# Optimization experiments

Measured on AMD Instinct MI355X. Metric: run time of the kernel, lower is better.

The kernel has to match this reference:

```python
import jax, jax.numpy as jnp
import numpy as np


def setup_inputs() -> dict:
    key = jax.random.key(0)
    ks = jax.random.split(key, 8)
    B, C, H, W = 8, 512, 64, 64
    Cr = C // 8  # reduction=8
    s = 1.0 / np.sqrt(C)
    return {
        "x": jax.random.normal(ks[0], (B, C, H, W), jnp.float32),
        "wq": jax.random.normal(ks[1], (Cr, C), jnp.float32) * s,
        "bq": jax.random.normal(ks[2], (Cr,), jnp.float32) * 0.01,
        "wk": jax.random.normal(ks[3], (Cr, C), jnp.float32) * s,
        "bk": jax.random.normal(ks[4], (Cr,), jnp.float32) * 0.01,
        "wv": jax.random.normal(ks[5], (C, C), jnp.float32) * s,
        "bv": jax.random.normal(ks[6], (C,), jnp.float32) * 0.01,
        "gamma": jax.random.normal(ks[7], (1,), jnp.float32),
    }


def reference(x, wq, bq, wk, bk, wv, bv, gamma):
    B, C, H, W = x.shape
    N = H * W
    xf = x.reshape(B, C, N)  # 1x1 conv == channel matmul
    q = jnp.einsum('qc,bcn->bnq', wq, xf) + bq  # [B, N, Cr]
    k = jnp.einsum('qc,bcn->bqn', wk, xf) + bk[None, :, None]  # [B, Cr, N]
    v = jnp.einsum('vc,bcn->bvn', wv, xf) + bv[None, :, None]  # [B, C, N]
    energy = jnp.einsum('bnq,bqm->bnm', q, k)  # [B, N, N]
    attn = jax.nn.softmax(energy, axis=-1)
    out = jnp.einsum('bcm,bnm->bcn', v, attn)  # [B, C, N]
    out = out.reshape(B, C, H, W)
    return gamma * out + x
```

## Files before the change

kernel.cpp:

```cpp
#include <hip/hip_runtime.h>

typedef float  f32x4  __attribute__((ext_vector_type(4)));
typedef float  f32x16 __attribute__((ext_vector_type(16)));
typedef short  short8 __attribute__((ext_vector_type(8)));
typedef unsigned int uint4v __attribute__((ext_vector_type(4)));

#define LOG2E 1.4426950408889634f
#define NPIX 4096
#define CCH  512
#define DQK  64

__device__ __forceinline__ ushort f2b(float f) {
  union { float f; unsigned u; } v; v.f = f;
  unsigned r = v.u + 0x7fffu + ((v.u >> 16) & 1u);
  return (ushort)(r >> 16);
}

__device__ __forceinline__ unsigned cvt_pk_bf16(float lo, float hi) {
  unsigned r;
  asm("v_cvt_pk_bf16_f32 %0, %1, %2" : "=v"(r) : "v"(lo), "v"(hi));
  return r;
}

__device__ __forceinline__ void plane_swap(unsigned &a, unsigned &b) {
  asm volatile("v_permlane32_swap_b32 %0, %1" : "+v"(a), "+v"(b));
}

__device__ __forceinline__ void gload16(const ushort* g, ushort* l) {
  __builtin_amdgcn_global_load_lds((const __attribute__((address_space(1))) void*)g,
                                   (__attribute__((address_space(3))) void*)l, 16, 0, 0);
}

__global__ __launch_bounds__(256) void k_cast_x(const float* __restrict__ x,
                                                ushort* __restrict__ Xt) {
  __shared__ float tile[32][33];
  const int b = blockIdx.z;
  const int n0 = blockIdx.x * 32, c0 = blockIdx.y * 32;
  const int t = threadIdx.x;
  {
    int cc = t >> 3, nn = (t & 7) * 4;
    const float4 v = *(const float4*)&x[((size_t)b * CCH + c0 + cc) * NPIX + n0 + nn];
    tile[cc][nn] = v.x; tile[cc][nn + 1] = v.y; tile[cc][nn + 2] = v.z; tile[cc][nn + 3] = v.w;
  }
  __syncthreads();
  {
    int nr = t >> 3, c4 = (t & 7) * 4;
    ushort4 o;
    o.x = f2b(tile[c4 + 0][nr]); o.y = f2b(tile[c4 + 1][nr]);
    o.z = f2b(tile[c4 + 2][nr]); o.w = f2b(tile[c4 + 3][nr]);
    *(ushort4*)&Xt[((size_t)b * NPIX + n0 + nr) * CCH + c0 + c4] = o;
  }
}

__global__ __launch_bounds__(256) void k_cast_w(const float* __restrict__ wq,
                                                const float* __restrict__ wk,
                                                const float* __restrict__ wv,
                                                ushort* __restrict__ Wb) {
  int i = blockIdx.x * 256 + threadIdx.x;
  int idx = i * 4;
  int j = idx >> 9, c = idx & 511;
  const float* src = (j < 64) ? &wq[(size_t)j * 512]
                   : (j < 128) ? &wk[(size_t)(j - 64) * 512]
                               : &wv[(size_t)(j - 128) * 512];
  float4 v = *(const float4*)&src[c];
  ushort4 o; o.x = f2b(v.x); o.y = f2b(v.y); o.z = f2b(v.z); o.w = f2b(v.w);
  *(ushort4*)&Wb[idx] = o;
}

__global__ __launch_bounds__(256) void k_proj(const ushort* __restrict__ Xt,
                                              const ushort* __restrict__ Wb,
                                              const float* __restrict__ bq,
                                              const float* __restrict__ bk,
                                              const float* __restrict__ bv,
                                              ushort* __restrict__ Qf,
                                              ushort* __restrict__ Kf,
                                              ushort* __restrict__ Vf) {
  __shared__ ushort Wl[64][72];
  __shared__ ushort Xl[64][72];
  const int b = blockIdx.z;
  const int n0 = blockIdx.x * 64;
  const int j0 = blockIdx.y * 64;
  const int t = threadIdx.x;
  const int w = t >> 6, l = t & 63;
  const int lr = l & 15, lq = l >> 4;
  const int wj = (w >> 1) * 32, wn = (w & 1) * 32;

  f32x4 acc[2][2];
#pragma unroll
  for (int a = 0; a < 2; ++a)
#pragma unroll
    for (int c = 0; c < 2; ++c) acc[a][c] = f32x4{0.f, 0.f, 0.f, 0.f};

  const int srow = t >> 2, sch = t & 3;
  for (int k0 = 0; k0 < 512; k0 += 64) {
    *(uint4*)&Wl[srow][sch * 8]       = *(const uint4*)&Wb[(size_t)(j0 + srow) * 512 + k0 + sch * 8];
    *(uint4*)&Wl[srow][(sch + 4) * 8] = *(const uint4*)&Wb[(size_t)(j0 + srow) * 512 + k0 + (sch + 4) * 8];
    *(uint4*)&Xl[srow][sch * 8]       = *(const uint4*)&Xt[((size_t)b * NPIX + n0 + srow) * 512 + k0 + sch * 8];
    *(uint4*)&Xl[srow][(sch + 4) * 8] = *(const uint4*)&Xt[((size_t)b * NPIX + n0 + srow) * 512 + k0 + (sch + 4) * 8];
    __syncthreads();
#pragma unroll
    for (int kt = 0; kt < 2; ++kt) {
      short8 af[2], bf[2];
#pragma unroll
      for (int jt = 0; jt < 2; ++jt)
        af[jt] = *(const short8*)&Wl[wj + jt * 16 + lr][kt * 32 + lq * 8];
#pragma unroll
      for (int nt = 0; nt < 2; ++nt)
        bf[nt] = *(const short8*)&Xl[wn + nt * 16 + lr][kt * 32 + lq * 8];
#pragma unroll
      for (int jt = 0; jt < 2; ++jt)
#pragma unroll
        for (int nt = 0; nt < 2; ++nt)
          acc[jt][nt] = __builtin_amdgcn_mfma_f32_16x16x32_bf16(af[jt], bf[nt], acc[jt][nt], 0, 0, 0);
    }
    __syncthreads();
  }

#pragma unroll
  for (int jt = 0; jt < 2; ++jt) {
    const int jb = j0 + wj + jt * 16;
#pragma unroll
    for (int nt = 0; nt < 2; ++nt) {
      const int n = n0 + wn + nt * 16 + lr;
      const int n32 = (n0 + wn) >> 5;
      if (jb < 64) {
        const int kd0 = jb + lq * 4;
        const int ks = jb >> 4;
        const int hl = lq >> 1;
        const int e0 = (lq * 4) & 7;
        const int lp = (nt * 16 + lr) + 32 * hl;
        ushort4 o;
        o.x = f2b(LOG2E * (acc[jt][nt][0] + bq[kd0 + 0]));
        o.y = f2b(LOG2E * (acc[jt][nt][1] + bq[kd0 + 1]));
        o.z = f2b(LOG2E * (acc[jt][nt][2] + bq[kd0 + 2]));
        o.w = f2b(LOG2E * (acc[jt][nt][3] + bq[kd0 + 3]));
        *(ushort4*)&Qf[((size_t)(b * 128 + n32) * 4 + ks) * 512 + lp * 8 + e0] = o;
      } else if (jb < 128) {
        const int kd0 = jb - 64 + lq * 4;
        const int ks = (jb - 64) >> 4;
        const int hl = lq >> 1;
        const int e0 = (lq * 4) & 7;
        const int lp = (nt * 16 + lr) + 32 * hl;
        ushort4 o;
        o.x = f2b(acc[jt][nt][0] + bk[kd0 + 0]);
        o.y = f2b(acc[jt][nt][1] + bk[kd0 + 1]);
        o.z = f2b(acc[jt][nt][2] + bk[kd0 + 2]);
        o.w = f2b(acc[jt][nt][3] + bk[kd0 + 3]);
        *(ushort4*)&Kf[((size_t)(b * 128 + n32) * 4 + ks) * 512 + lp * 8 + e0] = o;
      } else {
        const int kt = nt;
        const int hlv = (lr >> 3) & 1;
        const int e = lr & 7;
#pragma unroll
        for (int r = 0; r < 4; ++r) {
          const int c = jb - 128 + lq * 4 + r;
          Vf[(((size_t)(b * 128 + n32) * 16 + (c >> 5)) * 2 + kt) * 512 +
             (c & 31) * 8 + 256 * hlv + e] = f2b(acc[jt][nt][r] + bv[c]);
        }
      }
    }
  }
}

__global__ __launch_bounds__(512, 4) void k_attn(const ushort* __restrict__ Qf,
                                                 const ushort* __restrict__ Kf,
                                                 const ushort* __restrict__ Vf,
                                                 const float* __restrict__ x,
                                                 const float* __restrict__ gamma,
                                                 float* __restrict__ out) {
  __shared__ unsigned Plds[2][8][2][2][64][2];
  __shared__ ushort Klds[2][8192];
  __shared__ ushort Qlds[4096];
  __shared__ float Lred[2][4][32];
  const int id = blockIdx.x;
  const int b  = id & 7;
  const int qb = id >> 3;
  const int t = threadIdx.x;
  const int w = t >> 6, l = t & 63;
  const int lq = l & 31, h = l >> 5;
  const int kg = w >> 1;
  const int q32p = w & 1;
  const int qw = qb * 64;

  union PB { uint4v u; short8 s8; };

  const ushort* kslice = Kf + (size_t)(b * 128) * 2048;
  const ushort* vbase  = Vf + (size_t)b * 128 * 16384 + (size_t)(2 * w) * 1024 + (size_t)l * 8;

  f32x16 acc[2][2] = {};
  float Lp = 0.f;

  auto stageK = [&](int buf, int tile) {
    const ushort* src = kslice + (size_t)tile * 8192;
#pragma unroll
    for (int i = 0; i < 2; ++i) {
      const int cb_ = i * 512 + w * 64;
      gload16(src + (size_t)(cb_ + l) * 8, &Klds[buf][cb_ * 8]);
    }
  };

  gload16(Qf + (size_t)(b * 128 + qb * 2) * 2048 + (size_t)(w * 64 + l) * 8, &Qlds[w * 512]);
  stageK(0, 0);
  __syncthreads();

  for (int tile = 0; tile < 32; ++tile) {
    const int buf = tile & 1;
    if (tile + 1 < 32) stageK(buf ^ 1, tile + 1);

    {
      const ushort* kb = &Klds[buf][(kg * 4) * 512 + l * 8];
      short8 kf0 = *(const short8*)(kb);
      short8 kf1 = *(const short8*)(kb + 512);
      short8 kf2 = *(const short8*)(kb + 1024);
      short8 kf3 = *(const short8*)(kb + 1536);
      const ushort* qp = &Qlds[q32p * 2048 + l * 8];
      short8 q0 = *(const short8*)(qp);
      short8 q1 = *(const short8*)(qp + 512);
      short8 q2 = *(const short8*)(qp + 1024);
      short8 q3 = *(const short8*)(qp + 1536);
      f32x16 s = {};
      __builtin_amdgcn_s_setprio(1);
      s = __builtin_amdgcn_mfma_f32_32x32x16_bf16(kf0, q0, s, 0, 0, 0);
      s = __builtin_amdgcn_mfma_f32_32x32x16_bf16(kf1, q1, s, 0, 0, 0);
      s = __builtin_amdgcn_mfma_f32_32x32x16_bf16(kf2, q2, s, 0, 0, 0);
      s = __builtin_amdgcn_mfma_f32_32x32x16_bf16(kf3, q3, s, 0, 0, 0);
      __builtin_amdgcn_s_setprio(0);

      float sum = 0.f;
#pragma unroll
      for (int r = 0; r < 16; ++r) { s[r] = __builtin_amdgcn_exp2f(s[r]); sum += s[r]; }
      Lp += sum;
      unsigned pk0 = cvt_pk_bf16(s[0],  s[1]),  pk1 = cvt_pk_bf16(s[2],  s[3]);
      unsigned pk2 = cvt_pk_bf16(s[4],  s[5]),  pk3 = cvt_pk_bf16(s[6],  s[7]);
      unsigned pk4 = cvt_pk_bf16(s[8],  s[9]),  pk5 = cvt_pk_bf16(s[10], s[11]);
      unsigned pk6 = cvt_pk_bf16(s[12], s[13]), pk7 = cvt_pk_bf16(s[14], s[15]);
      plane_swap(pk0, pk2); plane_swap(pk1, pk3);
      plane_swap(pk4, pk6); plane_swap(pk5, pk7);
      *(uint2*)&Plds[buf][kg * 2 + 0][q32p][0][l][0] = uint2{pk0, pk1};
      *(uint2*)&Plds[buf][kg * 2 + 0][q32p][1][l][0] = uint2{pk2, pk3};
      *(uint2*)&Plds[buf][kg * 2 + 1][q32p][0][l][0] = uint2{pk4, pk5};
      *(uint2*)&Plds[buf][kg * 2 + 1][q32p][1][l][0] = uint2{pk6, pk7};
    }
    __syncthreads();

#pragma unroll
    for (int k8 = 0; k8 < 8; ++k8) {
      const ushort* pv = vbase + (size_t)(tile * 4 + (k8 >> 1)) * 16384 + (size_t)(k8 & 1) * 512;
      short8 v0 = *(const short8*)(pv);
      short8 v1 = *(const short8*)(pv + 1024);
      uint2 a0 = *(const uint2*)&Plds[buf][k8][0][0][l][0];
      uint2 a1 = *(const uint2*)&Plds[buf][k8][0][1][l][0];
      uint2 b0 = *(const uint2*)&Plds[buf][k8][1][0][l][0];
      uint2 b1 = *(const uint2*)&Plds[buf][k8][1][1][l][0];
      PB B0, B1;
      B0.u[0] = a0.x; B0.u[1] = a0.y; B0.u[2] = a1.x; B0.u[3] = a1.y;
      B1.u[0] = b0.x; B1.u[1] = b0.y; B1.u[2] = b1.x; B1.u[3] = b1.y;
      __builtin_amdgcn_s_setprio(1);
      acc[0][0] = __builtin_amdgcn_mfma_f32_32x32x16_bf16(v0, B0.s8, acc[0][0], 0, 0, 0);
      acc[0][1] = __builtin_amdgcn_mfma_f32_32x32x16_bf16(v1, B0.s8, acc[0][1], 0, 0, 0);
      acc[1][0] = __builtin_amdgcn_mfma_f32_32x32x16_bf16(v0, B1.s8, acc[1][0], 0, 0, 0);
      acc[1][1] = __builtin_amdgcn_mfma_f32_32x32x16_bf16(v1, B1.s8, acc[1][1], 0, 0, 0);
      __builtin_amdgcn_s_setprio(0);
    }
  }

  Lp += __shfl_xor(Lp, 32);
  Lred[q32p][kg][lq] = Lp;
  __syncthreads();
  float Lt0 = (Lred[0][0][lq] + Lred[0][1][lq]) + (Lred[0][2][lq] + Lred[0][3][lq]);
  float Lt1 = (Lred[1][0][lq] + Lred[1][1][lq]) + (Lred[1][2][lq] + Lred[1][3][lq]);
  const float g = gamma[0];
  const float gi0 = g / Lt0, gi1 = g / Lt1;
#pragma unroll
  for (int ct = 0; ct < 2; ++ct)
#pragma unroll
    for (int r = 0; r < 16; ++r) {
      const int c = w * 64 + ct * 32 + (r & 3) + 8 * (r >> 2) + 4 * h;
      const size_t base = ((size_t)b * CCH + c) * NPIX + qw + lq;
      out[base]      = gi0 * acc[0][ct][r] + x[base];
      out[base + 32] = gi1 * acc[1][ct][r] + x[base + 32];
    }
}

extern "C" void kernel_launch(void* const* d_in, const int* in_sizes, int n_in,
                              void* d_out, int out_size, void* d_ws, size_t ws_size,
                              hipStream_t stream) {
  const float* x     = (const float*)d_in[0];
  const float* wq    = (const float*)d_in[1];
  const float* bq    = (const float*)d_in[2];
  const float* wk    = (const float*)d_in[3];
  const float* bk    = (const float*)d_in[4];
  const float* wv    = (const float*)d_in[5];
  const float* bv    = (const float*)d_in[6];
  const float* gamma = (const float*)d_in[7];
  float* out = (float*)d_out;

  ushort* Xt = (ushort*)d_out;
  ushort* Wb = (ushort*)d_ws;
  ushort* Qf = Wb + (size_t)640 * 512;
  ushort* Kf = Qf + (size_t)8 * 128 * 4 * 512;
  ushort* Vf = Kf + (size_t)8 * 128 * 4 * 512;

  k_cast_x<<<dim3(NPIX / 32, CCH / 32, 8), 256, 0, stream>>>(x, Xt);
  k_cast_w<<<(640 * 512 / 4) / 256, 256, 0, stream>>>(wq, wk, wv, Wb);
  k_proj<<<dim3(NPIX / 64, 640 / 64, 8), 256, 0, stream>>>(Xt, Wb, bq, bk, bv, Qf, Kf, Vf);
  k_attn<<<dim3(512), 512, 0, stream>>>(Qf, Kf, Vf, x, gamma, out);
}
```

Before: 255.6 us.

## Double attention query tile per block to 128 with 1024-thread blocks

Each attention block now covers 128 queries with 16 waves instead of 64 queries with 8 waves, and the grid is halved to 256 blocks. Each wave now computes a 32-channel by 128-query output tile from a single V fragment load per step, instead of a 64-by-64 tile. The aim is to halve global V traffic and amortise K tile staging over twice as many queries. In exchange, LDS use for P and Q doubles and only one large block fits per CU, so register pressure and per-block synchronisation cost may rise.

```diff
diff --git a/kernel.cpp b/kernel.cpp
--- a/kernel.cpp
+++ b/kernel.cpp
@@ -162,44 +162,39 @@
   }
 }
 
-__global__ __launch_bounds__(512, 4) void k_attn(const ushort* __restrict__ Qf,
-                                                 const ushort* __restrict__ Kf,
-                                                 const ushort* __restrict__ Vf,
-                                                 const float* __restrict__ x,
-                                                 const float* __restrict__ gamma,
-                                                 float* __restrict__ out) {
-  __shared__ unsigned Plds[2][8][2][2][64][2];
+__global__ __launch_bounds__(1024, 4) void k_attn(const ushort* __restrict__ Qf,
+                                                  const ushort* __restrict__ Kf,
+                                                  const ushort* __restrict__ Vf,
+                                                  const float* __restrict__ x,
+                                                  const float* __restrict__ gamma,
+                                                  float* __restrict__ out) {
+  __shared__ unsigned Plds[2][8][4][2][64][2];
   __shared__ ushort Klds[2][8192];
-  __shared__ ushort Qlds[4096];
-  __shared__ float Lred[2][4][32];
+  __shared__ ushort Qlds[8192];
+  __shared__ float Lred[4][4][32];
   const int id = blockIdx.x;
   const int b  = id & 7;
   const int qb = id >> 3;
   const int t = threadIdx.x;
   const int w = t >> 6, l = t & 63;
   const int lq = l & 31, h = l >> 5;
-  const int kg = w >> 1;
-  const int q32p = w & 1;
-  const int qw = qb * 64;
+  const int kg = w >> 2;
+  const int q32p = w & 3;
+  const int qw = qb * 128;
 
   union PB { uint4v u; short8 s8; };
 
   const ushort* kslice = Kf + (size_t)(b * 128) * 2048;
-  const ushort* vbase  = Vf + (size_t)b * 128 * 16384 + (size_t)(2 * w) * 1024 + (size_t)l * 8;
-
-  f32x16 acc[2][2] = {};
+  const ushort* vbase  = Vf + (size_t)b * 128 * 16384 + (size_t)w * 1024 + (size_t)l * 8;
+
+  f32x16 acc[4] = {};
   float Lp = 0.f;
 
   auto stageK = [&](int buf, int tile) {
-    const ushort* src = kslice + (size_t)tile * 8192;
-#pragma unroll
-    for (int i = 0; i < 2; ++i) {
-      const int cb_ = i * 512 + w * 64;
-      gload16(src + (size_t)(cb_ + l) * 8, &Klds[buf][cb_ * 8]);
-    }
+    gload16(kslice + (size_t)tile * 8192 + (size_t)(w * 64 + l) * 8, &Klds[buf][w * 512]);
   };
 
-  gload16(Qf + (size_t)(b * 128 + qb * 2) * 2048 + (size_t)(w * 64 + l) * 8, &Qlds[w * 512]);
+  gload16(Qf + (size_t)(b * 128 + qb * 4) * 2048 + (size_t)(w * 64 + l) * 8, &Qlds[w * 512]);
   stageK(0, 0);
   __syncthreads();
 
@@ -208,7 +203,7 @@
     if (tile + 1 < 32) stageK(buf ^ 1, tile + 1);
 
     {
-      const ushort* kb = &Klds[buf][(kg * 4) * 512 + l * 8];
+      const ushort* kb = &Klds[buf][kg * 2048 + l * 8];
       short8 kf0 = *(const short8*)(kb);
       short8 kf1 = *(const short8*)(kb + 512);
       short8 kf2 = *(const short8*)(kb + 1024);
@@ -246,20 +241,25 @@
 #pragma unroll
     for (int k8 = 0; k8 < 8; ++k8) {
       const ushort* pv = vbase + (size_t)(tile * 4 + (k8 >> 1)) * 16384 + (size_t)(k8 & 1) * 512;
-      short8 v0 = *(const short8*)(pv);
-      short8 v1 = *(const short8*)(pv + 1024);
+      short8 v = *(const short8*)(pv);
       uint2 a0 = *(const uint2*)&Plds[buf][k8][0][0][l][0];
       uint2 a1 = *(const uint2*)&Plds[buf][k8][0][1][l][0];
       uint2 b0 = *(const uint2*)&Plds[buf][k8][1][0][l][0];
       uint2 b1 = *(const uint2*)&Plds[buf][k8][1][1][l][0];
-      PB B0, B1;
+      uint2 c0 = *(const uint2*)&Plds[buf][k8][2][0][l][0];
+      uint2 c1 = *(const uint2*)&Plds[buf][k8][2][1][l][0];
+      uint2 d0 = *(const uint2*)&Plds[buf][k8][3][0][l][0];
+      uint2 d1 = *(const uint2*)&Plds[buf][k8][3][1][l][0];
+      PB B0, B1, B2, B3;
       B0.u[0] = a0.x; B0.u[1] = a0.y; B0.u[2] = a1.x; B0.u[3] = a1.y;
       B1.u[0] = b0.x; B1.u[1] = b0.y; B1.u[2] = b1.x; B1.u[3] = b1.y;
+      B2.u[0] = c0.x; B2.u[1] = c0.y; B2.u[2] = c1.x; B2.u[3] = c1.y;
+      B3.u[0] = d0.x; B3.u[1] = d0.y; B3.u[2] = d1.x; B3.u[3] = d1.y;
       __builtin_amdgcn_s_setprio(1);
-      acc[0][0] = __builtin_amdgcn_mfma_f32_32x32x16_bf16(v0, B0.s8, acc[0][0], 0, 0, 0);
-      acc[0][1] = __builtin_amdgcn_mfma_f32_32x32x16_bf16(v1, B0.s8, acc[0][1], 0, 0, 0);
-      acc[1][0] = __builtin_amdgcn_mfma_f32_32x32x16_bf16(v0, B1.s8, acc[1][0], 0, 0, 0);
-      acc[1][1] = __builtin_amdgcn_mfma_f32_32x32x16_bf16(v1, B1.s8, acc[1][1], 0, 0, 0);
+      acc[0] = __builtin_amdgcn_mfma_f32_32x32x16_bf16(v, B0.s8, acc[0], 0, 0, 0);
+      acc[1] = __builtin_amdgcn_mfma_f32_32x32x16_bf16(v, B1.s8, acc[1], 0, 0, 0);
+      acc[2] = __builtin_amdgcn_mfma_f32_32x32x16_bf16(v, B2.s8, acc[2], 0, 0, 0);
+      acc[3] = __builtin_amdgcn_mfma_f32_32x32x16_bf16(v, B3.s8, acc[3], 0, 0, 0);
       __builtin_amdgcn_s_setprio(0);
     }
   }
@@ -267,19 +267,19 @@
   Lp += __shfl_xor(Lp, 32);
   Lred[q32p][kg][lq] = Lp;
   __syncthreads();
-  float Lt0 = (Lred[0][0][lq] + Lred[0][1][lq]) + (Lred[0][2][lq] + Lred[0][3][lq]);
-  float Lt1 = (Lred[1][0][lq] + Lred[1][1][lq]) + (Lred[1][2][lq] + Lred[1][3][lq]);
+  float Lt[4];
+#pragma unroll
+  for (int q32 = 0; q32 < 4; ++q32)
+    Lt[q32] = (Lred[q32][0][lq] + Lred[q32][1][lq]) + (Lred[q32][2][lq] + Lred[q32][3][lq]);
   const float g = gamma[0];
-  const float gi0 = g / Lt0, gi1 = g / Lt1;
-#pragma unroll
-  for (int ct = 0; ct < 2; ++ct)
-#pragma unroll
-    for (int r = 0; r < 16; ++r) {
-      const int c = w * 64 + ct * 32 + (r & 3) + 8 * (r >> 2) + 4 * h;
-      const size_t base = ((size_t)b * CCH + c) * NPIX + qw + lq;
-      out[base]      = gi0 * acc[0][ct][r] + x[base];
-      out[base + 32] = gi1 * acc[1][ct][r] + x[base + 32];
-    }
+#pragma unroll
+  for (int r = 0; r < 16; ++r) {
+    const int c = w * 32 + (r & 3) + 8 * (r >> 2) + 4 * h;
+    const size_t base = ((size_t)b * CCH + c) * NPIX + qw + lq;
+#pragma unroll
+    for (int q32 = 0; q32 < 4; ++q32)
+      out[base + q32 * 32] = (g / Lt[q32]) * acc[q32][r] + x[base + q32 * 32];
+  }
 }
 
 extern "C" void kernel_launch(void* const* d_in, const int* in_sizes, int n_in,
@@ -304,5 +304,5 @@
   k_cast_x<<<dim3(NPIX / 32, CCH / 32, 8), 256, 0, stream>>>(x, Xt);
   k_cast_w<<<(640 * 512 / 4) / 256, 256, 0, stream>>>(wq, wk, wv, Wb);
   k_proj<<<dim3(NPIX / 64, 640 / 64, 8), 256, 0, stream>>>(Xt, Wb, bq, bk, bv, Qf, Kf, Vf);
-  k_attn<<<dim3(512), 512, 0, stream>>>(Qf, Kf, Vf, x, gamma, out);
-}
+  k_attn<<<dim3(256), 1024, 0, stream>>>(Qf, Kf, Vf, x, gamma, out);
+}
```

After: 241.1 us. 1.06x faster.
